# Kernel optimization log

Hardware: AMD Instinct MI355X
Metric: run time of the kernel (lower is better)

Reference implementation:

```python
import jax, jax.numpy as jnp
import numpy as np

B, S = 2, 1024          # 2 sequences of 1024 tokens (prefill)
HID = 2880
HQ, HKV, D = 64, 8, 64  # query heads, kv heads, head_dim
W = 128                 # sliding window size
THETA = 150000.0
SCALE = D ** -0.5
Q_SIZE, KV_SIZE = HQ * D, HKV * D


def _rope_neox(pos, x):
    # pos: [T] int, x: [T, H, D] -> neox-style full-dim rotary
    half = D // 2
    inv_freq = 1.0 / (THETA ** (jnp.arange(half, dtype=jnp.float32) * 2.0 / D))
    ang = pos.astype(jnp.float32)[:, None] * inv_freq          # [T, D/2]
    cos = jnp.cos(ang)[:, None, :]                             # [T, 1, D/2]
    sin = jnp.sin(ang)[:, None, :]
    x1, x2 = x[..., :half], x[..., half:]
    return jnp.concatenate([x1 * cos - x2 * sin, x1 * sin + x2 * cos], axis=-1)


def setup_inputs() -> dict:
    key = jax.random.key(0)
    ks = jax.random.split(key, 10)
    s = 0.02
    hidden_states = jax.random.normal(ks[0], (B * S, HID), dtype=jnp.float32)
    positions = jnp.tile(jnp.arange(S, dtype=jnp.int32), B)    # per-sequence positions
    Wq = jax.random.normal(ks[1], (HID, Q_SIZE), dtype=jnp.float32) * s
    bq = jax.random.normal(ks[2], (Q_SIZE,), dtype=jnp.float32) * s
    Wk = jax.random.normal(ks[3], (HID, KV_SIZE), dtype=jnp.float32) * s
    bk = jax.random.normal(ks[4], (KV_SIZE,), dtype=jnp.float32) * s
    Wv = jax.random.normal(ks[5], (HID, KV_SIZE), dtype=jnp.float32) * s
    bv = jax.random.normal(ks[6], (KV_SIZE,), dtype=jnp.float32) * s
    Wo = jax.random.normal(ks[7], (Q_SIZE, HID), dtype=jnp.float32) * s
    bo = jax.random.normal(ks[8], (HID,), dtype=jnp.float32) * s
    return {"hidden_states": hidden_states, "positions": positions,
            "Wq": Wq, "bq": bq, "Wk": Wk, "bk": bk,
            "Wv": Wv, "bv": bv, "Wo": Wo, "bo": bo}


def reference(hidden_states, positions, Wq, bq, Wk, bk, Wv, bv, Wo, bo):
    T = hidden_states.shape[0]
    q = (hidden_states @ Wq + bq).reshape(T, HQ, D)
    k = (hidden_states @ Wk + bk).reshape(T, HKV, D)
    v = (hidden_states @ Wv + bv).reshape(T, HKV, D)
    q = _rope_neox(positions, q)
    k = _rope_neox(positions, k)

    # sliding-window causal attention (banded, window = last W keys + self)
    G = HQ // HKV  # GQA group size
    q5 = q.reshape(B, S, HKV, G, D)
    k4 = k.reshape(B, S, HKV, D)
    v4 = v.reshape(B, S, HKV, D)
    offs = jnp.arange(W + 1)
    idx = jnp.arange(S)[:, None] - W + offs[None, :]           # [S, W+1] key index j
    valid = idx >= 0                                           # causal+window band
    idx_c = jnp.clip(idx, 0, S - 1)
    kw = k4[:, idx_c]                                          # [B, S, W+1, HKV, D]
    vw = v4[:, idx_c]
    scores = jnp.einsum('bikgd,biwkd->bikgw', q5, kw) * SCALE  # [B,S,HKV,G,W+1]
    scores = jnp.where(valid[None, :, None, None, :], scores, jnp.float32(-1e30))
    p = jax.nn.softmax(scores, axis=-1)
    o = jnp.einsum('bikgw,biwkd->bikgd', p, vw).reshape(T, Q_SIZE)
    return o @ Wo + bo


if __name__ == '__main__':
    out = reference(**setup_inputs())
    print(out.shape, out.dtype)
```

## Files before the change

### kernel.cpp

```cpp
#include <hip/hip_runtime.h>

#define T_TOK 2048
#define S_LEN 1024
#define HIDN  2880
#define NHQ   64
#define NHKV  8
#define DH    64
#define QSZ   4096
#define KVSZ  512
#define WIN   128
#define NQKV  5120
#define NOPAD 2944
#define NT    45
#define NTO   64

typedef __attribute__((ext_vector_type(4))) float f32x4;
typedef __attribute__((ext_vector_type(8))) short bf16x8;
typedef __attribute__((ext_vector_type(4))) short s16x4;

__device__ __forceinline__ unsigned short f2bf(float f) {
  unsigned u = __float_as_uint(f);
  u += 0x7fffu + ((u >> 16) & 1u);
  return (unsigned short)(u >> 16);
}
__device__ __forceinline__ float bf2f(unsigned short s) {
  return __uint_as_float(((unsigned)s) << 16);
}
__device__ __forceinline__ void ld_g2l16(const void* g, void* l) {
  __builtin_amdgcn_global_load_lds(
      (const __attribute__((address_space(1))) unsigned int*)g,
      (__attribute__((address_space(3))) unsigned int*)l, 16, 0, 0);
}

#define NB_CONV 2880
#define NB_WQ   5760
#define NB_WK   720

__device__ __forceinline__ void transpose_tile(
    const float* __restrict__ W, unsigned short* __restrict__ WT,
    int N, int lbid, float (*tile)[72])
{
  const int tid = threadIdx.x;
  const int nbx = N >> 6;
  const int nb = (lbid % nbx) * 64;
  const int kb = (lbid / nbx) * 32;
  const int kk = tid >> 3;
  const int n8 = (tid & 7) * 8;
  const float* src = W + (size_t)(kb + kk) * N + nb + n8;
  *(f32x4*)&tile[kk][n8]     = *(const f32x4*)(src);
  *(f32x4*)&tile[kk][n8 + 4] = *(const f32x4*)(src + 4);
  __syncthreads();
  const int n  = tid & 63;
  const int k8 = (tid >> 6) * 8;
  bf16x8 p;
  #pragma unroll
  for (int j = 0; j < 8; ++j) p[j] = (short)f2bf(tile[k8 + j][n]);
  *(bf16x8*)(WT + (size_t)(nb + n) * HIDN + kb + k8) = p;
}

__global__ __launch_bounds__(256) void prep_kernel(
    const float* __restrict__ hidden, unsigned short* __restrict__ hbf,
    const float* __restrict__ Wq, const float* __restrict__ Wk,
    const float* __restrict__ Wv, unsigned short* __restrict__ WT)
{
  __shared__ float tile[32][72];
  const int bid = blockIdx.x;
  if (bid < NB_CONV) {
    const size_t off = ((size_t)bid * 256 + threadIdx.x) * 8;
    const f32x4 a = *(const f32x4*)(hidden + off);
    const f32x4 b = *(const f32x4*)(hidden + off + 4);
    bf16x8 p;
    p[0] = (short)f2bf(a[0]); p[1] = (short)f2bf(a[1]);
    p[2] = (short)f2bf(a[2]); p[3] = (short)f2bf(a[3]);
    p[4] = (short)f2bf(b[0]); p[5] = (short)f2bf(b[1]);
    p[6] = (short)f2bf(b[2]); p[7] = (short)f2bf(b[3]);
    *(bf16x8*)(hbf + off) = p;
  } else if (bid < NB_CONV + NB_WQ) {
    transpose_tile(Wq, WT, QSZ, bid - NB_CONV, tile);
  } else if (bid < NB_CONV + NB_WQ + NB_WK) {
    transpose_tile(Wk, WT + (size_t)QSZ * HIDN, KVSZ,
                   bid - NB_CONV - NB_WQ, tile);
  } else {
    transpose_tile(Wv, WT + (size_t)(QSZ + KVSZ) * HIDN, KVSZ,
                   bid - NB_CONV - NB_WQ - NB_WK, tile);
  }
}

__global__ __launch_bounds__(256) void transpose_w(
    const float* __restrict__ W, unsigned short* __restrict__ WT,
    int K, int N)
{
  __shared__ float tile[32][72];
  const int tid = threadIdx.x;
  const int nb = blockIdx.x * 64;
  const int kb = blockIdx.y * 32;
  const int kk = tid >> 3;
  const int n8 = (tid & 7) * 8;
  if (nb + 64 <= N) {
    const float* src = W + (size_t)(kb + kk) * N + nb + n8;
    *(f32x4*)&tile[kk][n8]     = *(const f32x4*)(src);
    *(f32x4*)&tile[kk][n8 + 4] = *(const f32x4*)(src + 4);
  } else {
    #pragma unroll
    for (int u = 0; u < 8; ++u)
      tile[kk][n8 + u] = (nb + n8 + u < N)
          ? W[(size_t)(kb + kk) * N + nb + n8 + u] : 0.f;
  }
  __syncthreads();
  const int n  = tid & 63;
  const int k8 = (tid >> 6) * 8;
  bf16x8 p;
  #pragma unroll
  for (int j = 0; j < 8; ++j) p[j] = (short)f2bf(tile[k8 + j][n]);
  *(bf16x8*)(WT + (size_t)(nb + n) * K + kb + k8) = p;
}

__device__ __forceinline__ void rope_epilogue8(
    f32x4 (*acc)[4], const float* __restrict__ bias,
    const int* __restrict__ pos, unsigned short* __restrict__ outp,
    int outStride, int colbase, int rowbase, int lane)
{
  const int fr = lane & 15;
  const int r4 = (lane >> 4) * 4;
  const float invf0 = exp2f((float)fr        * (-17.19460283f / 32.0f));
  const float invf1 = exp2f((float)(fr + 16) * (-17.19460283f / 32.0f));
  #pragma unroll
  for (int mt = 0; mt < 8; ++mt) {
    #pragma unroll
    for (int i = 0; i < 4; ++i) {
      const int m = rowbase + mt * 16 + r4 + i;
      const float p = (float)pos[m];
      #pragma unroll
      for (int ntp = 0; ntp < 2; ++ntp) {
        float sv, cv;
        __sincosf(p * (ntp ? invf1 : invf0), &sv, &cv);
        const int c1 = colbase + ntp * 16 + fr;
        const float x1 = acc[mt][ntp][i]     + bias[c1];
        const float x2 = acc[mt][ntp + 2][i] + bias[c1 + 32];
        outp[(size_t)m * outStride + c1]      = f2bf(x1 * cv - x2 * sv);
        outp[(size_t)m * outStride + c1 + 32] = f2bf(x1 * sv + x2 * cv);
      }
    }
  }
}

__global__ __launch_bounds__(512, 2) void gemm_qkv(
    const unsigned short* __restrict__ A, const unsigned short* __restrict__ BT,
    const float* __restrict__ bq, const float* __restrict__ bk,
    const float* __restrict__ bv, const int* __restrict__ pos,
    unsigned short* __restrict__ qb, unsigned short* __restrict__ kb,
    unsigned short* __restrict__ vT,
    const float* __restrict__ Wo, unsigned short* __restrict__ WoT)
{
  __shared__ unsigned short lds[65536];
  const int tid  = threadIdx.x;
  const int bid  = blockIdx.x;

  if (bid >= 160) {
    const int t2   = (bid - 160) * 2 + (tid >> 8);
    const int ltid = tid & 255;
    float* fb = (float*)lds;
    float (*tile)[72] = (float (*)[72])(fb + (tid >> 8) * (32 * 72));
    const int nb = (t2 % 46) * 64;
    const int kb = (t2 / 46) * 32;
    const int kk = ltid >> 3;
    const int n8 = (ltid & 7) * 8;
    if (nb + 64 <= HIDN) {
      const float* src = Wo + (size_t)(kb + kk) * HIDN + nb + n8;
      *(f32x4*)&tile[kk][n8]     = *(const f32x4*)(src);
      *(f32x4*)&tile[kk][n8 + 4] = *(const f32x4*)(src + 4);
    } else {
      #pragma unroll
      for (int u = 0; u < 8; ++u)
        tile[kk][n8 + u] = (nb + n8 + u < HIDN)
            ? Wo[(size_t)(kb + kk) * HIDN + nb + n8 + u] : 0.f;
    }
    __syncthreads();
    const int n  = ltid & 63;
    const int k8 = (ltid >> 6) * 8;
    bf16x8 p;
    #pragma unroll
    for (int j = 0; j < 8; ++j) p[j] = (short)f2bf(tile[k8 + j][n]);
    *(bf16x8*)(WoT + (size_t)(nb + n) * QSZ + kb + k8) = p;
    return;
  }

  const int lane = tid & 63;
  const int wid  = tid >> 6;
  const int wm   = wid >> 2;
  const int wn   = wid & 3;
  const int wg   = (bid & 7) * 20 + (bid >> 3);
  const int n0   = (wg % 20) * 256;
  const int m0   = (wg / 20) * 256;
  const int fr = lane & 15;
  const int fq = lane >> 4;

  const int rsub = tid >> 3;
  const int cg   = (tid & 7) ^ (rsub & 7);
  const unsigned short* Asrc = A  + (size_t)(m0 + rsub) * HIDN + cg * 8;
  const unsigned short* Bsrc = BT + (size_t)(n0 + rsub) * HIDN + cg * 8;
  const size_t half_step = (size_t)128 * HIDN;
  const size_t r64 = (size_t)64 * HIDN;

  #define STAGE(src, slot)                                         \
    do {                                                           \
      ld_g2l16((src),       (slot) + (size_t)tid * 8);             \
      ld_g2l16((src) + r64, (slot) + (size_t)(512 + tid) * 8);     \
    } while (0)

  STAGE(Bsrc,                  lds + 16384);
  STAGE(Bsrc + half_step,      lds + 24576);
  STAGE(Asrc,                  lds + 0);
  STAGE(Asrc + half_step,      lds + 8192);
  STAGE(Bsrc + 64,             lds + 32768 + 16384);
  STAGE(Bsrc + half_step + 64, lds + 32768 + 24576);
  STAGE(Asrc + 64,             lds + 32768 + 0);
  STAGE(Asrc + half_step + 64, lds + 32768 + 8192);
  asm volatile("s_waitcnt vmcnt(8)" ::: "memory");
  __builtin_amdgcn_s_barrier();

  f32x4 acc[8][4];
  #pragma unroll
  for (int i = 0; i < 8; ++i)
    #pragma unroll
    for (int j = 0; j < 4; ++j) acc[i][j] = (f32x4){0.f, 0.f, 0.f, 0.f};
  bf16x8 bfr[4][2];

  for (int t = 0; t < NT; ++t) {
    unsigned short* Abuf = lds + (t & 1) * 32768;
    unsigned short* Bbuf = Abuf + 16384;
    unsigned short* nAbuf = lds + ((t + 1) & 1) * 32768;
    const int kA = (t + 1) * 64;
    const int kB = (t + 2) * 64;
    #pragma unroll
    for (int q = 0; q < 4; ++q) {
      if (q == 0) {
        #pragma unroll
        for (int nf = 0; nf < 4; ++nf)
          #pragma unroll
          for (int ks = 0; ks < 2; ++ks) {
            const int R = wn * 64 + nf * 16 + fr;
            const int kc = ks * 4 + fq;
            bfr[nf][ks] = *(const bf16x8*)(Bbuf + R * 64 + ((kc ^ (R & 7)) << 3));
          }
      }
      bf16x8 af[2][2];
      #pragma unroll
      for (int j = 0; j < 2; ++j)
        #pragma unroll
        for (int ks = 0; ks < 2; ++ks) {
          const int R = wm * 128 + (q * 2 + j) * 16 + fr;
          const int kc = ks * 4 + fq;
          af[j][ks] = *(const bf16x8*)(Abuf + R * 64 + ((kc ^ (R & 7)) << 3));
        }
      if (q == 0) {
        if (t >= 1 && t <= NT - 2) STAGE(Asrc + kA, nAbuf);
      } else if (q == 1) {
        if (t >= 1 && t <= NT - 2) STAGE(Asrc + half_step + kA, nAbuf + 8192);
      } else if (q == 2) {
        if (t <= NT - 3) STAGE(Bsrc + kB, Bbuf);
      } else {
        if (t <= NT - 3) STAGE(Bsrc + half_step + kB, Bbuf + 8192);
      }
      if (q == 3) {
        if (t < NT - 2)       asm volatile("s_waitcnt vmcnt(4)" ::: "memory");
        else if (t == NT - 2) asm volatile("s_waitcnt vmcnt(0)" ::: "memory");
      }
      __builtin_amdgcn_s_barrier();
      __builtin_amdgcn_s_setprio(1);
      #pragma unroll
      for (int j = 0; j < 2; ++j)
        #pragma unroll
        for (int nf = 0; nf < 4; ++nf)
          #pragma unroll
          for (int ks = 0; ks < 2; ++ks)
            acc[q * 2 + j][nf] = __builtin_amdgcn_mfma_f32_16x16x32_bf16(
                af[j][ks], bfr[nf][ks], acc[q * 2 + j][nf], 0, 0, 0);
      __builtin_amdgcn_s_setprio(0);
      __builtin_amdgcn_s_barrier();
    }
  }
  #undef STAGE

  const int cb = n0 + wn * 64;
  const int rowbase = m0 + wm * 128;
  if (cb < QSZ) {
    rope_epilogue8(acc, bq, pos, qb, QSZ, cb, rowbase, lane);
  } else if (cb < QSZ + KVSZ) {
    rope_epilogue8(acc, bk, pos, kb, KVSZ, cb - QSZ, rowbase, lane);
  } else {
    const int r4 = (lane >> 4) * 4;
    #pragma unroll
    for (int nt = 0; nt < 4; ++nt) {
      const int vrow = cb - (QSZ + KVSZ) + nt * 16 + fr;
      const float bvv = bv[vrow];
      #pragma unroll
      for (int mt = 0; mt < 8; ++mt) {
        const int mb = rowbase + mt * 16 + r4;
        s16x4 p;
        p[0] = (short)f2bf(acc[mt][nt][0] + bvv);
        p[1] = (short)f2bf(acc[mt][nt][1] + bvv);
        p[2] = (short)f2bf(acc[mt][nt][2] + bvv);
        p[3] = (short)f2bf(acc[mt][nt][3] + bvv);
        *(s16x4*)(vT + (size_t)vrow * T_TOK + mb) = p;
      }
    }
  }
}

__global__ __launch_bounds__(512, 2) void gemm_o(
    const unsigned short* __restrict__ A, const unsigned short* __restrict__ BT,
    const float* __restrict__ bias, float* __restrict__ C)
{
  __shared__ unsigned short lds[65536];
  const int tid  = threadIdx.x;
  const int lane = tid & 63;
  const int wid  = tid >> 6;
  const int wm   = wid >> 1;
  const int wn   = wid & 1;
  const int bid  = blockIdx.x;
  const int wg   = (bid & 7) * 23 + (bid >> 3);
  const int m0   = (wg / 23) * 256;
  const int n0   = (wg % 23) * 128;
  const int fr = lane & 15;
  const int fq = lane >> 4;

  const int rsub = tid >> 3;
  const int cg   = (tid & 7) ^ (rsub & 7);
  const unsigned short* Asrc = A  + (size_t)(m0 + rsub) * QSZ + cg * 8;
  const unsigned short* Bsrc = BT + (size_t)(n0 + rsub) * QSZ + cg * 8;
  const size_t r64 = (size_t)64 * QSZ;

  #define STA(t, r)  ld_g2l16(Asrc + (size_t)(t) * 64 + (size_t)(r) * r64,   \
      lds + ((t) % 3) * 16384 + ((size_t)(r) * 512 + tid) * 8)
  #define STB(t, r)  ld_g2l16(Bsrc + (size_t)(t) * 64 + (size_t)(r) * r64,   \
      lds + 49152 + ((t) & 1) * 8192 + ((size_t)(r) * 512 + tid) * 8)

  STA(0, 0); STA(0, 1); STA(0, 2); STA(0, 3);
  STB(0, 0); STB(0, 1);
  STA(1, 0); STA(1, 1); STA(1, 2); STA(1, 3);
  STB(1, 0); STB(1, 1);
  asm volatile("s_waitcnt vmcnt(6)" ::: "memory");
  __builtin_amdgcn_s_barrier();

  f32x4 acc[4][4];
  #pragma unroll
  for (int i = 0; i < 4; ++i)
    #pragma unroll
    for (int j = 0; j < 4; ++j) acc[i][j] = (f32x4){0.f, 0.f, 0.f, 0.f};
  bf16x8 bfr[4][2];

  for (int t = 0; t < NTO; ++t) {
    unsigned short* Abuf = lds + (t % 3) * 16384;
    unsigned short* Bbuf = lds + 49152 + (t & 1) * 8192;
    #pragma unroll
    for (int nf = 0; nf < 4; ++nf)
      #pragma unroll
      for (int ks = 0; ks < 2; ++ks) {
        const int R = wn * 64 + nf * 16 + fr;
        const int kc = ks * 4 + fq;
        bfr[nf][ks] = *(const bf16x8*)(Bbuf + R * 64 + ((kc ^ (R & 7)) << 3));
      }
    bf16x8 af0[2][2];
    #pragma unroll
    for (int j = 0; j < 2; ++j)
      #pragma unroll
      for (int ks = 0; ks < 2; ++ks) {
        const int R = wm * 64 + j * 16 + fr;
        const int kc = ks * 4 + fq;
        af0[j][ks] = *(const bf16x8*)(Abuf + R * 64 + ((kc ^ (R & 7)) << 3));
      }
    if (t <= NTO - 3) { STA(t + 2, 0); STA(t + 2, 1); STA(t + 2, 2); STA(t + 2, 3); }
    __builtin_amdgcn_s_barrier();
    __builtin_amdgcn_s_setprio(1);
    #pragma unroll
    for (int j = 0; j < 2; ++j)
      #pragma unroll
      for (int nf = 0; nf < 4; ++nf)
        #pragma unroll
        for (int ks = 0; ks < 2; ++ks)
          acc[j][nf] = __builtin_amdgcn_mfma_f32_16x16x32_bf16(
              af0[j][ks], bfr[nf][ks], acc[j][nf], 0, 0, 0);
    __builtin_amdgcn_s_setprio(0);
    __builtin_amdgcn_s_barrier();
    bf16x8 af1[2][2];
    #pragma unroll
    for (int j = 0; j < 2; ++j)
      #pragma unroll
      for (int ks = 0; ks < 2; ++ks) {
        const int R = wm * 64 + (2 + j) * 16 + fr;
        const int kc = ks * 4 + fq;
        af1[j][ks] = *(const bf16x8*)(Abuf + R * 64 + ((kc ^ (R & 7)) << 3));
      }
    if (t <= NTO - 3) { STB(t + 2, 0); STB(t + 2, 1); }
    if (t <= NTO - 3)      asm volatile("s_waitcnt vmcnt(6)" ::: "memory");
    else if (t == NTO - 2) asm volatile("s_waitcnt vmcnt(0)" ::: "memory");
    __builtin_amdgcn_s_barrier();
    __builtin_amdgcn_s_setprio(1);
    #pragma unroll
    for (int j = 0; j < 2; ++j)
      #pragma unroll
      for (int nf = 0; nf < 4; ++nf)
        #pragma unroll
        for (int ks = 0; ks < 2; ++ks)
          acc[2 + j][nf] = __builtin_amdgcn_mfma_f32_16x16x32_bf16(
              af1[j][ks], bfr[nf][ks], acc[2 + j][nf], 0, 0, 0);
    __builtin_amdgcn_s_setprio(0);
    __builtin_amdgcn_s_barrier();
  }
  #undef STA
  #undef STB

  const int r4 = (lane >> 4) * 4;
  #pragma unroll
  for (int nt = 0; nt < 4; ++nt) {
    const int n = n0 + wn * 64 + nt * 16 + fr;
    if (n >= HIDN) continue;
    const float bvv = bias[n];
    #pragma unroll
    for (int mt = 0; mt < 4; ++mt) {
      const int mb = m0 + wm * 64 + mt * 16 + r4;
      #pragma unroll
      for (int i = 0; i < 4; ++i)
        C[(size_t)(mb + i) * HIDN + n] = acc[mt][nt][i] + bvv;
    }
  }
}

__global__ __launch_bounds__(256, 3) void attn_kernel(
    const unsigned short* __restrict__ q, const unsigned short* __restrict__ k,
    const unsigned short* __restrict__ vT, unsigned short* __restrict__ o)
{
  __shared__ unsigned short lds[26624];
  unsigned short* Ks = lds;
  unsigned short* Vt = lds;
  unsigned short* Ps = lds + 13824;

  const int tid  = threadIdx.x;
  const int lane = tid & 63;
  const int wid  = tid >> 6;
  const int sq0  = blockIdx.x * 64;
  const int hp   = blockIdx.y;
  const int b    = blockIdx.z;
  const int h0   = hp * 2;
  const int kvh  = hp >> 2;
  const int kp0  = sq0 - WIN;

  const int fr = lane & 15;
  const int fk = (lane >> 4) * 8;
  const int qw = wid * 16;

  bf16x8 qf[2][2];
  {
    const size_t qrow = (size_t)(b * S_LEN + sq0 + qw + fr) * QSZ;
    #pragma unroll
    for (int hh = 0; hh < 2; ++hh)
      #pragma unroll
      for (int ks2 = 0; ks2 < 2; ++ks2)
        qf[hh][ks2] = *(const bf16x8*)(q + qrow + (h0 + hh) * DH + ks2 * 32 + fk);
  }

  #pragma unroll
  for (int j = 0; j < 6; ++j) {
    const int c  = tid + j * 256;
    const int kr = c >> 3, dc = (c & 7) * 8;
    int tok = b * S_LEN + kp0 + kr;
    if (tok < 0) tok = 0;
    const bf16x8 vv = *(const bf16x8*)(k + (size_t)tok * KVSZ + kvh * DH + dc);
    *(bf16x8*)&Ks[kr * 72 + dc] = vv;
  }
  __syncthreads();

  f32x4 S0[12], S1[12];
  #pragma unroll
  for (int i = 0; i < 12; ++i) {
    S0[i] = (f32x4){0.f, 0.f, 0.f, 0.f};
    S1[i] = (f32x4){0.f, 0.f, 0.f, 0.f};
  }
  #pragma unroll
  for (int ks2 = 0; ks2 < 2; ++ks2) {
    #pragma unroll
    for (int nt = 0; nt < 12; ++nt) {
      const bf16x8 bfr = *(const bf16x8*)&Ks[(nt * 16 + fr) * 72 + ks2 * 32 + fk];
      S0[nt] = __builtin_amdgcn_mfma_f32_16x16x32_bf16(qf[0][ks2], bfr, S0[nt], 0, 0, 0);
      S1[nt] = __builtin_amdgcn_mfma_f32_16x16x32_bf16(qf[1][ks2], bfr, S1[nt], 0, 0, 0);
    }
  }

  const int qbase = sq0 + qw + ((lane >> 4) << 2);
  float ls0[4] = {0.f, 0.f, 0.f, 0.f};
  float ls1[4] = {0.f, 0.f, 0.f, 0.f};
  #pragma unroll
  for (int nt = 0; nt < 12; ++nt) {
    const int jpos = kp0 + nt * 16 + fr;
    #pragma unroll
    for (int i = 0; i < 4; ++i) {
      const int qa = qbase + i;
      const bool valid = (jpos >= 0) && (jpos <= qa) && (jpos >= qa - WIN);
      const float e0 = valid ? __expf(S0[nt][i] * 0.125f) : 0.f;
      const float e1 = valid ? __expf(S1[nt][i] * 0.125f) : 0.f;
      S0[nt][i] = e0; ls0[i] += e0;
      S1[nt][i] = e1; ls1[i] += e1;
    }
  }
  #pragma unroll
  for (int off = 1; off < 16; off <<= 1)
    #pragma unroll
    for (int i = 0; i < 4; ++i) {
      ls0[i] += __shfl_xor(ls0[i], off, 64);
      ls1[i] += __shfl_xor(ls1[i], off, 64);
    }
  float inv0[4], inv1[4];
  #pragma unroll
  for (int i = 0; i < 4; ++i) {
    inv0[i] = 1.0f / ls0[i];
    inv1[i] = 1.0f / ls1[i];
  }
  __syncthreads();

  #pragma unroll
  for (int nt = 0; nt < 12; ++nt)
    #pragma unroll
    for (int i = 0; i < 4; ++i)
      Ps[(qbase - sq0 + i) * 200 + nt * 16 + fr] = f2bf(S0[nt][i]);
  if (kp0 >= 0) {
    #pragma unroll
    for (int j = 0; j < 6; ++j) {
      const int c  = tid + j * 256;
      const int dr = c / 24, kc = (c % 24) * 8;
      const bf16x8 vv = *(const bf16x8*)(
          vT + (size_t)(kvh * DH + dr) * T_TOK + b * S_LEN + kp0 + kc);
      *(bf16x8*)&Vt[dr * 200 + kc] = vv;
    }
  } else {
    #pragma unroll
    for (int j = 0; j < 6; ++j) {
      const int c  = tid + j * 256;
      const int dr = c / 24, kc = (c % 24) * 8;
      bf16x8 vv;
      #pragma unroll
      for (int u = 0; u < 8; ++u) {
        int col = b * S_LEN + kp0 + kc + u;
        if (col < 0) col = 0;
        vv[u] = (short)vT[(size_t)(kvh * DH + dr) * T_TOK + col];
      }
      *(bf16x8*)&Vt[dr * 200 + kc] = vv;
    }
  }
  __syncthreads();

  {
    f32x4 O[4];
    #pragma unroll
    for (int i = 0; i < 4; ++i) O[i] = (f32x4){0.f, 0.f, 0.f, 0.f};
    #pragma unroll
    for (int ks2 = 0; ks2 < 6; ++ks2) {
      const bf16x8 pa = *(const bf16x8*)&Ps[(qw + fr) * 200 + ks2 * 32 + fk];
      #pragma unroll
      for (int nt = 0; nt < 4; ++nt) {
        const bf16x8 vb = *(const bf16x8*)&Vt[(nt * 16 + fr) * 200 + ks2 * 32 + fk];
        O[nt] = __builtin_amdgcn_mfma_f32_16x16x32_bf16(pa, vb, O[nt], 0, 0, 0);
      }
    }
    #pragma unroll
    for (int nt = 0; nt < 4; ++nt)
      #pragma unroll
      for (int i = 0; i < 4; ++i)
        o[(size_t)(b * S_LEN + qbase + i) * QSZ + h0 * DH + nt * 16 + fr] =
            f2bf(O[nt][i] * inv0[i]);
  }
  __syncthreads();

  #pragma unroll
  for (int nt = 0; nt < 12; ++nt)
    #pragma unroll
    for (int i = 0; i < 4; ++i)
      Ps[(qbase - sq0 + i) * 200 + nt * 16 + fr] = f2bf(S1[nt][i]);
  __syncthreads();

  {
    f32x4 O[4];
    #pragma unroll
    for (int i = 0; i < 4; ++i) O[i] = (f32x4){0.f, 0.f, 0.f, 0.f};
    #pragma unroll
    for (int ks2 = 0; ks2 < 6; ++ks2) {
      const bf16x8 pa = *(const bf16x8*)&Ps[(qw + fr) * 200 + ks2 * 32 + fk];
      #pragma unroll
      for (int nt = 0; nt < 4; ++nt) {
        const bf16x8 vb = *(const bf16x8*)&Vt[(nt * 16 + fr) * 200 + ks2 * 32 + fk];
        O[nt] = __builtin_amdgcn_mfma_f32_16x16x32_bf16(pa, vb, O[nt], 0, 0, 0);
      }
    }
    #pragma unroll
    for (int nt = 0; nt < 4; ++nt)
      #pragma unroll
      for (int i = 0; i < 4; ++i)
        o[(size_t)(b * S_LEN + qbase + i) * QSZ + (h0 + 1) * DH + nt * 16 + fr] =
            f2bf(O[nt][i] * inv1[i]);
  }
}

extern "C" void kernel_launch(void* const* d_in, const int* in_sizes, int n_in,
                              void* d_out, int out_size, void* d_ws, size_t ws_size,
                              hipStream_t stream) {
  const float* hidden    = (const float*)d_in[0];
  const int*   positions = (const int*)d_in[1];
  const float* Wq = (const float*)d_in[2];
  const float* bq = (const float*)d_in[3];
  const float* Wk = (const float*)d_in[4];
  const float* bk = (const float*)d_in[5];
  const float* Wv = (const float*)d_in[6];
  const float* bv = (const float*)d_in[7];
  const float* Wo = (const float*)d_in[8];
  const float* bo = (const float*)d_in[9];
  float* out = (float*)d_out;

  char* ws = (char*)d_ws;
  unsigned short* hbf   = (unsigned short*)(ws);
  unsigned short* WqkvT = (unsigned short*)(ws + 11796480);
  unsigned short* qb    = (unsigned short*)(ws + 41287680);
  unsigned short* kb    = (unsigned short*)(ws + 58064896);
  unsigned short* vTb   = (unsigned short*)(ws + 60162048);

  const bool merged = ws_size >= (size_t)86376448;
  unsigned short* WoT = merged ? (unsigned short*)(ws + 62259200) : WqkvT;

  prep_kernel<<<dim3(NB_CONV + NB_WQ + 2 * NB_WK), dim3(256), 0, stream>>>(
      hidden, hbf, Wq, Wk, Wv, WqkvT);

  if (merged) {
    gemm_qkv<<<dim3(160 + 2944), dim3(512), 0, stream>>>(
        hbf, WqkvT, bq, bk, bv, positions, qb, kb, vTb, Wo, WoT);
  } else {
    gemm_qkv<<<dim3(160), dim3(512), 0, stream>>>(
        hbf, WqkvT, bq, bk, bv, positions, qb, kb, vTb, Wo, WoT);
    transpose_w<<<dim3(NOPAD / 64, QSZ / 32), dim3(256), 0, stream>>>(
        Wo, WqkvT, QSZ, HIDN);
  }

  attn_kernel<<<dim3(S_LEN / 64, NHQ / 2, 2), dim3(256), 0, stream>>>(
      qb, kb, vTb, qb);
  gemm_o<<<dim3(184), dim3(512), 0, stream>>>(
      qb, WoT, bo, out);
}
```

Baseline: 328.8 us.

## Skip out-of-band score tiles in attention and batch Wo transpose into persistent blocks

In the attention kernel each wave now computes only the 9 key tiles that can overlap its 16-query band instead of all 12, and zero-fills the P tile that sits just outside that band. The PV product then runs 5 of the 6 k-steps, starting at an offset set by the wave. This removes masked QK^T and PV MFMAs and the exp work that goes with them. The Wo transpose blocks inside gemm_qkv drop from 2944 to 96, each looping over 31 tiles with register prefetch of the next tile, which cuts block launch overhead but lengthens the tail of that kernel.

```diff
diff --git a/kernel.cpp b/kernel.cpp
--- a/kernel.cpp
+++ b/kernel.cpp
@@ -157,31 +157,64 @@
   const int bid  = blockIdx.x;
 
   if (bid >= 160) {
-    const int t2   = (bid - 160) * 2 + (tid >> 8);
+    const int half = tid >> 8;
     const int ltid = tid & 255;
     float* fb = (float*)lds;
-    float (*tile)[72] = (float (*)[72])(fb + (tid >> 8) * (32 * 72));
-    const int nb = (t2 % 46) * 64;
-    const int kb = (t2 / 46) * 32;
+    float (*tile)[72] = (float (*)[72])(fb + half * (32 * 72));
+    const int slot = (bid - 160) * 2 + half;
     const int kk = ltid >> 3;
     const int n8 = (ltid & 7) * 8;
-    if (nb + 64 <= HIDN) {
-      const float* src = Wo + (size_t)(kb + kk) * HIDN + nb + n8;
-      *(f32x4*)&tile[kk][n8]     = *(const f32x4*)(src);
-      *(f32x4*)&tile[kk][n8 + 4] = *(const f32x4*)(src + 4);
-    } else {
-      #pragma unroll
-      for (int u = 0; u < 8; ++u)
-        tile[kk][n8 + u] = (nb + n8 + u < HIDN)
-            ? Wo[(size_t)(kb + kk) * HIDN + nb + n8 + u] : 0.f;
-    }
-    __syncthreads();
     const int n  = ltid & 63;
     const int k8 = (ltid >> 6) * 8;
-    bf16x8 p;
-    #pragma unroll
-    for (int j = 0; j < 8; ++j) p[j] = (short)f2bf(tile[k8 + j][n]);
-    *(bf16x8*)(WoT + (size_t)(nb + n) * QSZ + kb + k8) = p;
+    f32x4 va = {0.f, 0.f, 0.f, 0.f}, vb = {0.f, 0.f, 0.f, 0.f};
+    int nb = 0, kb2 = 0;
+    {
+      const int t2 = slot * 31;
+      if (t2 < 5888) {
+        nb = (t2 % 46) * 64; kb2 = (t2 / 46) * 32;
+        const float* src = Wo + (size_t)(kb2 + kk) * HIDN + nb + n8;
+        if (nb + 64 <= HIDN) {
+          va = *(const f32x4*)src; vb = *(const f32x4*)(src + 4);
+        } else {
+          #pragma unroll
+          for (int u = 0; u < 4; ++u) {
+            va[u] = (nb + n8 + u     < HIDN) ? src[u]     : 0.f;
+            vb[u] = (nb + n8 + 4 + u < HIDN) ? src[4 + u] : 0.f;
+          }
+        }
+      }
+    }
+    for (int it = 0; it < 31; ++it) {
+      const int t2 = slot * 31 + it;
+      const bool ok = t2 < 5888;
+      const int cnb = nb, ckb = kb2;
+      __syncthreads();
+      if (ok) {
+        *(f32x4*)&tile[kk][n8]     = va;
+        *(f32x4*)&tile[kk][n8 + 4] = vb;
+      }
+      __syncthreads();
+      const int t2n = t2 + 1;
+      if (it + 1 < 31 && t2n < 5888) {
+        nb = (t2n % 46) * 64; kb2 = (t2n / 46) * 32;
+        const float* src = Wo + (size_t)(kb2 + kk) * HIDN + nb + n8;
+        if (nb + 64 <= HIDN) {
+          va = *(const f32x4*)src; vb = *(const f32x4*)(src + 4);
+        } else {
+          #pragma unroll
+          for (int u = 0; u < 4; ++u) {
+            va[u] = (nb + n8 + u     < HIDN) ? src[u]     : 0.f;
+            vb[u] = (nb + n8 + 4 + u < HIDN) ? src[4 + u] : 0.f;
+          }
+        }
+      }
+      if (ok) {
+        bf16x8 p;
+        #pragma unroll
+        for (int j = 0; j < 8; ++j) p[j] = (short)f2bf(tile[k8 + j][n]);
+        *(bf16x8*)(WoT + (size_t)(cnb + n) * QSZ + ckb + k8) = p;
+      }
+    }
     return;
   }
 
@@ -449,6 +482,7 @@
   const int fr = lane & 15;
   const int fk = (lane >> 4) * 8;
   const int qw = wid * 16;
+  const int ntb = wid;
 
   bf16x8 qf[2][2];
   {
@@ -471,19 +505,20 @@
   }
   __syncthreads();
 
-  f32x4 S0[12], S1[12];
-  #pragma unroll
-  for (int i = 0; i < 12; ++i) {
+  f32x4 S0[9], S1[9];
+  #pragma unroll
+  for (int i = 0; i < 9; ++i) {
     S0[i] = (f32x4){0.f, 0.f, 0.f, 0.f};
     S1[i] = (f32x4){0.f, 0.f, 0.f, 0.f};
   }
   #pragma unroll
   for (int ks2 = 0; ks2 < 2; ++ks2) {
     #pragma unroll
-    for (int nt = 0; nt < 12; ++nt) {
-      const bf16x8 bfr = *(const bf16x8*)&Ks[(nt * 16 + fr) * 72 + ks2 * 32 + fk];
-      S0[nt] = __builtin_amdgcn_mfma_f32_16x16x32_bf16(qf[0][ks2], bfr, S0[nt], 0, 0, 0);
-      S1[nt] = __builtin_amdgcn_mfma_f32_16x16x32_bf16(qf[1][ks2], bfr, S1[nt], 0, 0, 0);
+    for (int j = 0; j < 9; ++j) {
+      const bf16x8 bfr =
+          *(const bf16x8*)&Ks[((ntb + j) * 16 + fr) * 72 + ks2 * 32 + fk];
+      S0[j] = __builtin_amdgcn_mfma_f32_16x16x32_bf16(qf[0][ks2], bfr, S0[j], 0, 0, 0);
+      S1[j] = __builtin_amdgcn_mfma_f32_16x16x32_bf16(qf[1][ks2], bfr, S1[j], 0, 0, 0);
     }
   }
 
@@ -491,16 +526,16 @@
   float ls0[4] = {0.f, 0.f, 0.f, 0.f};
   float ls1[4] = {0.f, 0.f, 0.f, 0.f};
   #pragma unroll
-  for (int nt = 0; nt < 12; ++nt) {
-    const int jpos = kp0 + nt * 16 + fr;
+  for (int j = 0; j < 9; ++j) {
+    const int jpos = kp0 + (ntb + j) * 16 + fr;
     #pragma unroll
     for (int i = 0; i < 4; ++i) {
       const int qa = qbase + i;
       const bool valid = (jpos >= 0) && (jpos <= qa) && (jpos >= qa - WIN);
-      const float e0 = valid ? __expf(S0[nt][i] * 0.125f) : 0.f;
-      const float e1 = valid ? __expf(S1[nt][i] * 0.125f) : 0.f;
-      S0[nt][i] = e0; ls0[i] += e0;
-      S1[nt][i] = e1; ls1[i] += e1;
+      const float e0 = valid ? __expf(S0[j][i] * 0.125f) : 0.f;
+      const float e1 = valid ? __expf(S1[j][i] * 0.125f) : 0.f;
+      S0[j][i] = e0; ls0[i] += e0;
+      S1[j][i] = e1; ls1[i] += e1;
     }
   }
   #pragma unroll
@@ -519,10 +554,16 @@
   __syncthreads();
 
   #pragma unroll
-  for (int nt = 0; nt < 12; ++nt)
+  for (int j = 0; j < 9; ++j)
     #pragma unroll
     for (int i = 0; i < 4; ++i)
-      Ps[(qbase - sq0 + i) * 200 + nt * 16 + fr] = f2bf(S0[nt][i]);
+      Ps[(qbase - sq0 + i) * 200 + (ntb + j) * 16 + fr] = f2bf(S0[j][i]);
+  {
+    const int zt = (wid & 1) ? (wid - 1) : (wid + 9);
+    #pragma unroll
+    for (int i = 0; i < 4; ++i)
+      Ps[(qbase - sq0 + i) * 200 + zt * 16 + fr] = 0;
+  }
   if (kp0 >= 0) {
     #pragma unroll
     for (int j = 0; j < 6; ++j) {
@@ -549,12 +590,14 @@
   }
   __syncthreads();
 
+  const int ks0 = wid >> 1;
   {
     f32x4 O[4];
     #pragma unroll
     for (int i = 0; i < 4; ++i) O[i] = (f32x4){0.f, 0.f, 0.f, 0.f};
     #pragma unroll
-    for (int ks2 = 0; ks2 < 6; ++ks2) {
+    for (int kq = 0; kq < 5; ++kq) {
+      const int ks2 = ks0 + kq;
       const bf16x8 pa = *(const bf16x8*)&Ps[(qw + fr) * 200 + ks2 * 32 + fk];
       #pragma unroll
       for (int nt = 0; nt < 4; ++nt) {
@@ -572,10 +615,10 @@
   __syncthreads();
 
   #pragma unroll
-  for (int nt = 0; nt < 12; ++nt)
+  for (int j = 0; j < 9; ++j)
     #pragma unroll
     for (int i = 0; i < 4; ++i)
-      Ps[(qbase - sq0 + i) * 200 + nt * 16 + fr] = f2bf(S1[nt][i]);
+      Ps[(qbase - sq0 + i) * 200 + (ntb + j) * 16 + fr] = f2bf(S1[j][i]);
   __syncthreads();
 
   {
@@ -583,7 +626,8 @@
     #pragma unroll
     for (int i = 0; i < 4; ++i) O[i] = (f32x4){0.f, 0.f, 0.f, 0.f};
     #pragma unroll
-    for (int ks2 = 0; ks2 < 6; ++ks2) {
+    for (int kq = 0; kq < 5; ++kq) {
+      const int ks2 = ks0 + kq;
       const bf16x8 pa = *(const bf16x8*)&Ps[(qw + fr) * 200 + ks2 * 32 + fk];
       #pragma unroll
       for (int nt = 0; nt < 4; ++nt) {
@@ -629,7 +673,7 @@
       hidden, hbf, Wq, Wk, Wv, WqkvT);
 
   if (merged) {
-    gemm_qkv<<<dim3(160 + 2944), dim3(512), 0, stream>>>(
+    gemm_qkv<<<dim3(256), dim3(512), 0, stream>>>(
         hbf, WqkvT, bq, bk, bv, positions, qb, kb, vTb, Wo, WoT);
   } else {
     gemm_qkv<<<dim3(160), dim3(512), 0, stream>>>(
```

Measured after the change: 331.2 us. Within noise of the previous version (+0.7%).
